# Performance work log

Hardware: AMD Instinct MI355X
Metric: run time of the kernel (lower is better)

## Reference

```python
import jax, jax.numpy as jnp
import numpy as np

D_MODEL = 1024
N_HEADS = 16
HEAD_DIM = D_MODEL // N_HEADS
ROPE_BASE = 10000.0
RMS_EPS = 1e-5


def setup_inputs() -> dict:
    key = jax.random.key(0)
    k1, k2, k3 = jax.random.split(key, 3)
    B, T = 2, 2048
    x = jax.random.normal(k1, (B, T, D_MODEL), dtype=jnp.float32)
    norm_w = jnp.ones((D_MODEL,), dtype=jnp.float32)
    w_qkv = jax.random.normal(k2, (3 * D_MODEL, D_MODEL), dtype=jnp.float32) * (D_MODEL ** -0.5)
    w_out = jax.random.normal(k3, (D_MODEL, D_MODEL), dtype=jnp.float32) * (D_MODEL ** -0.5)
    return {"x": x, "norm_w": norm_w, "w_qkv": w_qkv, "w_out": w_out}


def _rope_cos_sin(T, dtype):
    inv_freq = 1.0 / (ROPE_BASE ** (jnp.arange(0, HEAD_DIM, 2, dtype=jnp.float32) / HEAD_DIM))
    t = jnp.arange(T, dtype=jnp.float32)
    freqs = t[:, None] * inv_freq[None, :]            # [T, HEAD_DIM//2]
    emb = jnp.concatenate([freqs, freqs], axis=-1)    # [T, HEAD_DIM]
    return jnp.cos(emb).astype(dtype), jnp.sin(emb).astype(dtype)


def _rotate_half(x):
    x1, x2 = jnp.split(x, 2, axis=-1)
    return jnp.concatenate([-x2, x1], axis=-1)


def reference(x, norm_w, w_qkv, w_out):
    B, T, _ = x.shape
    residual = x
    # RMSNorm
    rms = jax.lax.rsqrt(jnp.mean(x * x, axis=-1, keepdims=True) + RMS_EPS)
    xn = x * rms * norm_w
    # QKV projection (torch Linear: x @ W.T)
    qkv = xn @ w_qkv.T                                  # [B, T, 3*D]
    qkv = qkv.reshape(B, T, 3, N_HEADS, HEAD_DIM)
    q, k, v = qkv[:, :, 0], qkv[:, :, 1], qkv[:, :, 2]  # [B, T, H, hd]
    # RoPE on q, k
    cos, sin = _rope_cos_sin(T, q.dtype)                # [T, hd]
    cos = cos[None, :, None, :]
    sin = sin[None, :, None, :]
    q = q * cos + _rotate_half(q) * sin
    k = k * cos + _rotate_half(k) * sin
    # Bidirectional SDPA: [B, H, T, hd]
    qh = q.transpose(0, 2, 1, 3)
    kh = k.transpose(0, 2, 1, 3)
    vh = v.transpose(0, 2, 1, 3)
    scale = HEAD_DIM ** -0.5
    scores = jnp.einsum('bhqd,bhkd->bhqk', qh, kh) * scale
    attn = jax.nn.softmax(scores, axis=-1)
    out = jnp.einsum('bhqk,bhkd->bhqd', attn, vh)       # [B, H, T, hd]
    out = out.transpose(0, 2, 1, 3).reshape(B, T, D_MODEL)
    out = out @ w_out.T
    return residual + out
```

## Files before the change

kernel.cpp:

```cpp
#include <hip/hip_runtime.h>
#include <hip/hip_bf16.h>
#include <math.h>


typedef __bf16 bf16;
typedef __bf16 bf16x8 __attribute__((ext_vector_type(8)));
typedef __bf16 bf16x4 __attribute__((ext_vector_type(4)));
typedef float  f32x4  __attribute__((ext_vector_type(4)));
typedef unsigned u32x4 __attribute__((ext_vector_type(4)));

#define GLOAD16(g, l) __builtin_amdgcn_global_load_lds( \
    (const __attribute__((address_space(1))) void*)(g),  \
    (__attribute__((address_space(3))) void*)(l), 16, 0, 0)

__device__ __forceinline__ unsigned pk2(float a, float b) {
  unsigned short lo = __builtin_bit_cast(unsigned short, (bf16)a);
  unsigned short hi = __builtin_bit_cast(unsigned short, (bf16)b);
  return (unsigned)lo | ((unsigned)hi << 16);
}

__global__ __launch_bounds__(256) void k_cvt(const float* __restrict__ src,
    bf16* __restrict__ dst, int n) {
  int i = (blockIdx.x * 256 + threadIdx.x) * 8;
  if (i >= n) return;
  float4 a = *(const float4*)(src + i);
  float4 b = *(const float4*)(src + i + 4);
  bf16x8 o;
  o[0] = (bf16)a.x; o[1] = (bf16)a.y; o[2] = (bf16)a.z; o[3] = (bf16)a.w;
  o[4] = (bf16)b.x; o[5] = (bf16)b.y; o[6] = (bf16)b.z; o[7] = (bf16)b.w;
  *(bf16x8*)(dst + i) = o;
}

__global__ __launch_bounds__(256) void k_rmsnorm(const float* __restrict__ x,
    const float* __restrict__ w, bf16* __restrict__ xn) {
  const int row = blockIdx.x, tid = threadIdx.x;
  float4 v = *(const float4*)(x + (size_t)row * 1024 + tid * 4);
  float ss = v.x * v.x + v.y * v.y + v.z * v.z + v.w * v.w;
  for (int m = 32; m >= 1; m >>= 1) ss += __shfl_xor(ss, m);
  __shared__ float red[4];
  if ((tid & 63) == 0) red[tid >> 6] = ss;
  __syncthreads();
  float ms = (red[0] + red[1] + red[2] + red[3]) * (1.f / 1024.f);
  float r = rsqrtf(ms + 1e-5f);
  float4 wv = *(const float4*)(w + tid * 4);
  bf16x4 o;
  o[0] = (bf16)(v.x * r * wv.x); o[1] = (bf16)(v.y * r * wv.y);
  o[2] = (bf16)(v.z * r * wv.z); o[3] = (bf16)(v.w * r * wv.w);
  *(bf16x4*)(xn + (size_t)row * 1024 + tid * 4) = o;
}

template<int RESID>
__global__ __launch_bounds__(256, 2) void k_gemm_bt(const bf16* __restrict__ A,
    const bf16* __restrict__ B, const float* __restrict__ R, void* __restrict__ Cv,
    int M, int N, int K, int lda) {
  const int tid = threadIdx.x;
  const int lane = tid & 63, L15 = lane & 15, quad = lane >> 4;
  const int wave = tid >> 6, wr = wave >> 1, wc = wave & 1;
  const int n0 = blockIdx.x * 128, m0 = blockIdx.y * 128;
  __shared__ __align__(16) bf16 smem[17408];
  bf16* sA = smem; bf16* sB = smem + 8192;
  f32x4 acc[4][4];
  const f32x4 z = {0.f, 0.f, 0.f, 0.f};
  for (int i = 0; i < 4; i++) for (int j = 0; j < 4; j++) acc[i][j] = z;

  for (int k0 = 0; k0 < K; k0 += 64) {
    const bf16* Ab = A + (size_t)m0 * lda + k0;
    const bf16* Bb = B + (size_t)n0 * K + k0;
    for (int p = 0; p < 4; p++) {
      int s = p * 256 + tid, r = s >> 3, c8 = (s & 7) ^ (r & 7);
      GLOAD16(Ab + (size_t)r * lda + c8 * 8, sA + s * 8);
      GLOAD16(Bb + (size_t)r * K + c8 * 8, sB + s * 8);
    }
    __syncthreads();
    for (int kk = 0; kk < 2; kk++) {
      bf16x8 af[4], bfv[4];
      for (int i = 0; i < 4; i++) {
        int ra = wr * 64 + i * 16 + L15;
        af[i] = *(const bf16x8*)(sA + ra * 64 + (((kk * 4 + quad) ^ (ra & 7)) * 8));
        int rb = wc * 64 + i * 16 + L15;
        bfv[i] = *(const bf16x8*)(sB + rb * 64 + (((kk * 4 + quad) ^ (rb & 7)) * 8));
      }
      for (int mt = 0; mt < 4; mt++)
        for (int nt = 0; nt < 4; nt++)
          acc[mt][nt] = __builtin_amdgcn_mfma_f32_16x16x32_bf16(af[mt], bfv[nt], acc[mt][nt], 0, 0, 0);
    }
    __syncthreads();
  }
  bf16* sC = smem;
  for (int mt = 0; mt < 4; mt++) for (int nt = 0; nt < 4; nt++) {
    int r = wr * 64 + mt * 16 + quad * 4, c = wc * 64 + nt * 16 + L15;
    f32x4 v = acc[mt][nt];
    for (int g = 0; g < 4; g++) sC[(r + g) * 136 + c] = (bf16)v[g];
  }
  __syncthreads();
  const int rr = tid >> 1, sg = (tid & 1) * 64;
  const size_t row = (size_t)m0 + rr;
  const bf16* src = sC + rr * 136 + sg;
  if (RESID) {
    float* Cf = (float*)Cv;
    const float* rs = R + row * N + n0 + sg;
    float* dst = Cf + row * N + n0 + sg;
    for (int i = 0; i < 16; i++) {
      bf16x4 u = *(const bf16x4*)(src + i * 4);
      float4 rv = *(const float4*)(rs + i * 4);
      float4 o;
      o.x = (float)u[0] + rv.x; o.y = (float)u[1] + rv.y;
      o.z = (float)u[2] + rv.z; o.w = (float)u[3] + rv.w;
      *(float4*)(dst + i * 4) = o;
    }
  } else {
    bf16* Cb = (bf16*)Cv;
    bf16* dst = Cb + row * N + n0 + sg;
    for (int i = 0; i < 8; i++)
      *(bf16x8*)(dst + i * 8) = *(const bf16x8*)(src + i * 8);
  }
}

__global__ __launch_bounds__(256) void k_rope(bf16* __restrict__ qkv,
    bf16* __restrict__ vt) {
  const int blk = blockIdx.x;
  const int tt = blk & 31, h = (blk >> 5) & 15, b = blk >> 9;
  const int tid = threadIdx.x;
  const int bh = b * 16 + h;
  {
    const int tl = tid >> 2, dp = (tid & 3) * 8;
    const int tg = tt * 64 + tl;
    bf16* base = qkv + (size_t)(b * 2048 + tg) * 3072 + h * 64;
    bf16x8 qlo = *(const bf16x8*)(base + dp);
    bf16x8 qhi = *(const bf16x8*)(base + dp + 32);
    bf16x8 klo = *(const bf16x8*)(base + 1024 + dp);
    bf16x8 khi = *(const bf16x8*)(base + 1024 + dp + 32);
    bf16x8 oql, oqh, okl, okh;
    for (int j = 0; j < 8; j++) {
      float invf = exp2f(-0.41524101186f * (float)(dp + j));
      float th = (float)tg * invf;
      float sn, cs;
      sincosf(th, &sn, &cs);
      float a0 = (float)qlo[j], a1 = (float)qhi[j];
      float b0 = (float)klo[j], b1 = (float)khi[j];
      oql[j] = (bf16)(a0 * cs - a1 * sn);
      oqh[j] = (bf16)(a1 * cs + a0 * sn);
      okl[j] = (bf16)(b0 * cs - b1 * sn);
      okh[j] = (bf16)(b1 * cs + b0 * sn);
    }
    *(bf16x8*)(base + dp) = oql; *(bf16x8*)(base + dp + 32) = oqh;
    *(bf16x8*)(base + 1024 + dp) = okl; *(bf16x8*)(base + 1024 + dp + 32) = okh;
  }
  __shared__ __align__(16) bf16 sT[64 * 72];
  for (int p = 0; p < 2; p++) {
    int s = p * 256 + tid, tl = s >> 3, c = s & 7;
    const bf16* vsrc = qkv + (size_t)(b * 2048 + tt * 64 + tl) * 3072 + 2048 + h * 64 + c * 8;
    *(bf16x8*)(sT + tl * 72 + c * 8) = *(const bf16x8*)vsrc;
  }
  __syncthreads();
  for (int p = 0; p < 2; p++) {
    int s = p * 256 + tid, d = s >> 3, tc = s & 7;
    bf16x8 v;
    for (int j = 0; j < 8; j++) v[j] = sT[(tc * 8 + j) * 72 + d];
    *(bf16x8*)(vt + (size_t)bh * 131072 + (size_t)d * 2048 + tt * 64 + tc * 8) = v;
  }
}

__global__ __launch_bounds__(256, 3) void k_attn(bf16* __restrict__ qkv,
    const bf16* __restrict__ vt) {
  const int tid = threadIdx.x;
  const int lane = tid & 63, L15 = lane & 15, quad = lane >> 4;
  const int wave = tid >> 6;
  const int bh = blockIdx.y, b = bh >> 4, h = bh & 15;
  const int q0 = blockIdx.x * 128;
  const bf16* Q  = qkv + (size_t)b * 2048 * 3072 + h * 64;
  const bf16* Kg = qkv + (size_t)b * 2048 * 3072 + 1024 + h * 64;
  const bf16* Vg = vt + (size_t)bh * 131072;
  __shared__ __align__(16) bf16 smem[16384];
  bf16* sK = smem;
  bf16* sV = smem + 8192;

  bf16x8 qf[2][2];
  for (int qt = 0; qt < 2; qt++) for (int kk = 0; kk < 2; kk++) {
    int rq = q0 + wave * 32 + qt * 16 + L15;
    qf[qt][kk] = *(const bf16x8*)(Q + (size_t)rq * 3072 + kk * 32 + quad * 8);
  }
  f32x4 o[4][2];
  const f32x4 z = {0.f, 0.f, 0.f, 0.f};
  for (int i = 0; i < 4; i++) for (int j = 0; j < 2; j++) o[i][j] = z;
  float mrun[2] = {-1e30f, -1e30f};
  float lrun[2] = {0.f, 0.f};
  const float c2l = 0.125f * 1.44269504089f;

  for (int kv0 = 0; kv0 < 2048; kv0 += 128) {
    __syncthreads();
    const bf16* Kb = Kg + (size_t)kv0 * 3072;
    for (int p = 0; p < 4; p++) {
      int s = p * 256 + tid, r = s >> 3, c8 = (s & 7) ^ (r & 7);
      GLOAD16(Kb + (size_t)r * 3072 + c8 * 8, sK + s * 8);
    }
    for (int p = 0; p < 4; p++) {
      int s = p * 256 + tid, r = s >> 4, cl = s & 15;
      int c8 = (cl & 8) | ((cl ^ (r & 7)) & 7);
      GLOAD16(Vg + (size_t)r * 2048 + kv0 + c8 * 8, sV + s * 8);
    }
    __syncthreads();
    f32x4 st[8][2];
#pragma unroll
    for (int i = 0; i < 8; i++) for (int j = 0; j < 2; j++) st[i][j] = z;
#pragma unroll
    for (int kk = 0; kk < 2; kk++) {
      bf16x8 kf[8];
#pragma unroll
      for (int kvt = 0; kvt < 8; kvt++) {
        int rk = kvt * 16 + L15;
        kf[kvt] = *(const bf16x8*)(sK + rk * 64 + (((kk * 4 + quad) ^ (rk & 7)) * 8));
      }
#pragma unroll
      for (int kvt = 0; kvt < 8; kvt++)
        for (int qt = 0; qt < 2; qt++)
          st[kvt][qt] = __builtin_amdgcn_mfma_f32_16x16x32_bf16(kf[kvt], qf[qt][kk], st[kvt][qt], 0, 0, 0);
    }
    unsigned pA[2][8], pB[2][8];
#pragma unroll
    for (int qt = 0; qt < 2; qt++) {
      float m = st[0][qt][0];
#pragma unroll
      for (int kvt = 0; kvt < 8; kvt++)
        for (int g = 0; g < 4; g++) m = fmaxf(m, st[kvt][qt][g]);
      m = fmaxf(m, __shfl_xor(m, 16));
      m = fmaxf(m, __shfl_xor(m, 32));
      if (__any(m > mrun[qt] + 8.f)) {
        float mnew = fmaxf(mrun[qt], m);
        float alpha = __builtin_amdgcn_exp2f((mrun[qt] - mnew) * c2l);
        lrun[qt] *= alpha;
#pragma unroll
        for (int dt = 0; dt < 4; dt++) o[dt][qt] *= alpha;
        mrun[qt] = mnew;
      }
      float mc = mrun[qt] * c2l;
      float ls = 0.f;
#pragma unroll
      for (int kvt = 0; kvt < 8; kvt++) {
        float p0 = __builtin_amdgcn_exp2f(st[kvt][qt][0] * c2l - mc);
        float p1 = __builtin_amdgcn_exp2f(st[kvt][qt][1] * c2l - mc);
        float p2 = __builtin_amdgcn_exp2f(st[kvt][qt][2] * c2l - mc);
        float p3 = __builtin_amdgcn_exp2f(st[kvt][qt][3] * c2l - mc);
        ls += (p0 + p1) + (p2 + p3);
        pA[qt][kvt] = pk2(p0, p1);
        pB[qt][kvt] = pk2(p2, p3);
      }
      ls += __shfl_xor(ls, 16);
      ls += __shfl_xor(ls, 32);
      lrun[qt] += ls;
    }
#pragma unroll
    for (int kc = 0; kc < 4; kc++) {
      bf16x8 vf[4];
#pragma unroll
      for (int dt = 0; dt < 4; dt++) {
        int rd = dt * 16 + L15;
        int c = kc * 4 + quad;
        int cs = (c & 8) | ((c ^ (rd & 7)) & 7);
        vf[dt] = *(const bf16x8*)(sV + rd * 128 + cs * 8);
      }
#pragma unroll
      for (int qt = 0; qt < 2; qt++) {
        auto rA = __builtin_amdgcn_permlane32_swap(pA[qt][2 * kc], pA[qt][2 * kc + 1], false, false);
        auto tAC = __builtin_amdgcn_permlane16_swap(rA[0], rA[1], false, false);
        auto rB = __builtin_amdgcn_permlane32_swap(pB[qt][2 * kc], pB[qt][2 * kc + 1], false, false);
        auto tBD = __builtin_amdgcn_permlane16_swap(rB[0], rB[1], false, false);
        u32x4 pw;
        pw[0] = tAC[0]; pw[1] = tBD[0]; pw[2] = tAC[1]; pw[3] = tBD[1];
        bf16x8 pf = __builtin_bit_cast(bf16x8, pw);
#pragma unroll
        for (int dt = 0; dt < 4; dt++)
          o[dt][qt] = __builtin_amdgcn_mfma_f32_16x16x32_bf16(vf[dt], pf, o[dt][qt], 0, 0, 0);
      }
    }
  }
  float invl[2] = {1.f / lrun[0], 1.f / lrun[1]};
  __syncthreads();
  bf16* sO = smem;
  for (int dt = 0; dt < 4; dt++) for (int qt = 0; qt < 2; qt++) {
    f32x4 v = o[dt][qt] * invl[qt];
    int ql = wave * 32 + qt * 16 + L15;
    uint2 w2; w2.x = pk2(v[0], v[1]); w2.y = pk2(v[2], v[3]);
    *(uint2*)(sO + ql * 72 + dt * 16 + quad * 4) = w2;
  }
  __syncthreads();
  const int rr = tid >> 1, sg = (tid & 1) * 32;
  const bf16* src = sO + rr * 72 + sg;
  bf16* dst = qkv + (size_t)(b * 2048 + q0 + rr) * 3072 + h * 64 + sg;
  for (int i = 0; i < 4; i++)
    *(bf16x8*)(dst + i * 8) = *(const bf16x8*)(src + i * 8);
}

extern "C" void kernel_launch(void* const* d_in, const int* in_sizes, int n_in,
                              void* d_out, int out_size, void* d_ws, size_t ws_size,
                              hipStream_t stream) {
  (void)in_sizes; (void)n_in; (void)out_size;
  const float* x     = (const float*)d_in[0];
  const float* normw = (const float*)d_in[1];
  const float* wqkv  = (const float*)d_in[2];
  const float* wout  = (const float*)d_in[3];
  float* out = (float*)d_out;
  bf16* ws  = (bf16*)d_ws;
  const size_t NQKV = (size_t)4096 * 3072, NXN = (size_t)4096 * 1024;
  const size_t NWQ = (size_t)3072 * 1024, NWO = (size_t)1024 * 1024;
  const size_t need = (NQKV + NXN + NWQ + NWO) * sizeof(bf16);
  if (ws_size < need) return;
  bf16* qkv    = ws;
  bf16* xn     = qkv + NQKV;
  bf16* vtp    = xn;
  bf16* wqkvb  = xn + NXN;
  bf16* woutb  = wqkvb + NWQ;
  k_cvt<<<(int)(NWQ / 8 / 256), 256, 0, stream>>>(wqkv, wqkvb, (int)NWQ);
  k_cvt<<<(int)(NWO / 8 / 256), 256, 0, stream>>>(wout, woutb, (int)NWO);
  k_rmsnorm<<<4096, 256, 0, stream>>>(x, normw, xn);
  k_gemm_bt<0><<<dim3(24, 32), 256, 0, stream>>>(xn, wqkvb, nullptr, qkv, 4096, 3072, 1024, 1024);
  k_rope<<<1024, 256, 0, stream>>>(qkv, vtp);
  k_attn<<<dim3(16, 32), 256, 0, stream>>>(qkv, vtp);
  k_gemm_bt<1><<<dim3(8, 32), 256, 0, stream>>>(qkv, woutb, x, out, 4096, 1024, 1024, 3072);
}
```

Before: 219.4 us.

## Double-buffer K/V tiles in attention and compute row sums via MFMA

The attention kernel now keeps two LDS buffers for K/V tiles and prefetches the next tile with async global-to-LDS loads while computing on the current one, using explicit vmcnt waits and raw barriers. The softmax denominator is no longer summed with VALU adds and cross-lane shuffles. It is accumulated by an extra MFMA against a vector of ones, which also gives bf16-rounded sums consistent with the P used for the output. LDS use doubles and occupancy hint drops from 3 to 2 blocks per CU, trading parallelism for overlap of loads with compute.

New measurement: 211.8 us. 3.4% less time.

```diff
diff --git a/kernel.cpp b/kernel.cpp
--- a/kernel.cpp
+++ b/kernel.cpp
@@ -161,7 +161,7 @@
   }
 }
 
-__global__ __launch_bounds__(256, 3) void k_attn(bf16* __restrict__ qkv,
+__global__ __launch_bounds__(256, 2) void k_attn(bf16* __restrict__ qkv,
     const bf16* __restrict__ vt) {
   const int tid = threadIdx.x;
   const int lane = tid & 63, L15 = lane & 15, quad = lane >> 4;
@@ -171,9 +171,7 @@
   const bf16* Q  = qkv + (size_t)b * 2048 * 3072 + h * 64;
   const bf16* Kg = qkv + (size_t)b * 2048 * 3072 + 1024 + h * 64;
   const bf16* Vg = vt + (size_t)bh * 131072;
-  __shared__ __align__(16) bf16 smem[16384];
-  bf16* sK = smem;
-  bf16* sV = smem + 8192;
+  __shared__ __align__(16) bf16 smem[32768];
 
   bf16x8 qf[2][2];
   for (int qt = 0; qt < 2; qt++) for (int kk = 0; kk < 2; kk++) {
@@ -183,23 +181,41 @@
   f32x4 o[4][2];
   const f32x4 z = {0.f, 0.f, 0.f, 0.f};
   for (int i = 0; i < 4; i++) for (int j = 0; j < 2; j++) o[i][j] = z;
+  f32x4 o5[2] = {z, z};
+  const bf16 one = (bf16)1.0f;
+  const bf16x8 ones8 = {one, one, one, one, one, one, one, one};
   float mrun[2] = {-1e30f, -1e30f};
-  float lrun[2] = {0.f, 0.f};
   const float c2l = 0.125f * 1.44269504089f;
 
-  for (int kv0 = 0; kv0 < 2048; kv0 += 128) {
-    __syncthreads();
+  auto STAGE = [&](int kv0, int base) {
     const bf16* Kb = Kg + (size_t)kv0 * 3072;
+    bf16* sKb = smem + base;
+    bf16* sVb = smem + base + 8192;
     for (int p = 0; p < 4; p++) {
       int s = p * 256 + tid, r = s >> 3, c8 = (s & 7) ^ (r & 7);
-      GLOAD16(Kb + (size_t)r * 3072 + c8 * 8, sK + s * 8);
+      GLOAD16(Kb + (size_t)r * 3072 + c8 * 8, sKb + s * 8);
     }
     for (int p = 0; p < 4; p++) {
       int s = p * 256 + tid, r = s >> 4, cl = s & 15;
       int c8 = (cl & 8) | ((cl ^ (r & 7)) & 7);
-      GLOAD16(Vg + (size_t)r * 2048 + kv0 + c8 * 8, sV + s * 8);
-    }
-    __syncthreads();
+      GLOAD16(Vg + (size_t)r * 2048 + kv0 + c8 * 8, sVb + s * 8);
+    }
+  };
+
+  STAGE(0, 0);
+  for (int t = 0; t < 16; ++t) {
+    const int cur = (t & 1) << 14;
+    if (t < 15) {
+      STAGE((t + 1) << 7, cur ^ 16384);
+      asm volatile("s_waitcnt vmcnt(8)" ::: "memory");
+    } else {
+      asm volatile("s_waitcnt vmcnt(0)" ::: "memory");
+    }
+    __builtin_amdgcn_s_barrier();
+    __builtin_amdgcn_sched_barrier(0);
+    const bf16* sK = smem + cur;
+    const bf16* sV = smem + cur + 8192;
+
     f32x4 st[8][2];
 #pragma unroll
     for (int i = 0; i < 8; i++) for (int j = 0; j < 2; j++) st[i][j] = z;
@@ -228,26 +244,21 @@
       if (__any(m > mrun[qt] + 8.f)) {
         float mnew = fmaxf(mrun[qt], m);
         float alpha = __builtin_amdgcn_exp2f((mrun[qt] - mnew) * c2l);
-        lrun[qt] *= alpha;
 #pragma unroll
         for (int dt = 0; dt < 4; dt++) o[dt][qt] *= alpha;
+        o5[qt] *= alpha;
         mrun[qt] = mnew;
       }
       float mc = mrun[qt] * c2l;
-      float ls = 0.f;
 #pragma unroll
       for (int kvt = 0; kvt < 8; kvt++) {
         float p0 = __builtin_amdgcn_exp2f(st[kvt][qt][0] * c2l - mc);
         float p1 = __builtin_amdgcn_exp2f(st[kvt][qt][1] * c2l - mc);
         float p2 = __builtin_amdgcn_exp2f(st[kvt][qt][2] * c2l - mc);
         float p3 = __builtin_amdgcn_exp2f(st[kvt][qt][3] * c2l - mc);
-        ls += (p0 + p1) + (p2 + p3);
         pA[qt][kvt] = pk2(p0, p1);
         pB[qt][kvt] = pk2(p2, p3);
       }
-      ls += __shfl_xor(ls, 16);
-      ls += __shfl_xor(ls, 32);
-      lrun[qt] += ls;
     }
 #pragma unroll
     for (int kc = 0; kc < 4; kc++) {
@@ -271,11 +282,14 @@
 #pragma unroll
         for (int dt = 0; dt < 4; dt++)
           o[dt][qt] = __builtin_amdgcn_mfma_f32_16x16x32_bf16(vf[dt], pf, o[dt][qt], 0, 0, 0);
-      }
-    }
-  }
-  float invl[2] = {1.f / lrun[0], 1.f / lrun[1]};
-  __syncthreads();
+        o5[qt] = __builtin_amdgcn_mfma_f32_16x16x32_bf16(ones8, pf, o5[qt], 0, 0, 0);
+      }
+    }
+    asm volatile("s_waitcnt lgkmcnt(0)" ::: "memory");
+    __builtin_amdgcn_sched_barrier(0);
+    __builtin_amdgcn_s_barrier();
+  }
+  float invl[2] = {1.f / o5[0][0], 1.f / o5[1][0]};
   bf16* sO = smem;
   for (int dt = 0; dt < 4; dt++) for (int qt = 0; qt < 2; qt++) {
     f32x4 v = o[dt][qt] * invl[qt];
```
